# Performance work log

Hardware: AMD Instinct MI355X
Metric: run time of the kernel (lower is better)

Reference implementation:

```python
import jax, jax.numpy as jnp
import numpy as np

D = 4096          # input_dim == output_dim (square FAUST factors)
N = 1024          # batch rows of U
NNZ = 131072      # nonzeros per factor (32 per row)
K = 4             # number of sparse factors


def setup_inputs() -> dict:
    key = jax.random.key(0)
    k_u, k_b, k_v, k_r, k_c = jax.random.split(key, 5)
    U = jax.random.normal(k_u, (N, D), dtype=jnp.float32)
    bias = jax.random.normal(k_b, (D,), dtype=jnp.float32)
    # glorot-ish scaling: ~32 nnz per row -> scale by 1/sqrt(32) for stable chain
    vals = jax.random.normal(k_v, (K, NNZ), dtype=jnp.float32) * (1.0 / np.sqrt(32.0))
    rows = jax.random.randint(k_r, (K, NNZ), 0, D, dtype=jnp.int32)
    cols = jax.random.randint(k_c, (K, NNZ), 0, D, dtype=jnp.int32)
    return {"U": U, "bias": bias, "vals": vals, "rows": rows, "cols": cols}


def _spmm(rows, cols, vals, X):
    # sparse (COO) [D, D] @ dense X [D, N] -> [D, N]
    return jax.ops.segment_sum(vals[:, None] * X[cols], rows, num_segments=D)


def reference(U, bias, vals, rows, cols):
    # torch code applies sparse_matrices[-1] first, then [k-2] ... [0]
    y = U.T  # [D, N]
    for i in range(K - 1, -1, -1):
        y = _spmm(rows[i], cols[i], vals[i], y)
    return y.T + bias  # [N, D]
```

## Files before the change

### kernel.cpp

```cpp
#include <hip/hip_runtime.h>

#define D_DIM 4096
#define N_DIM 1024
#define NNZ_F 131072
#define K_F 4
#define NCHUNK 8
#define LPR 16
#define RPB 16
#define MAXE 1024
#define XS8 (N_DIM / 8)

#define T_TILES ((D_DIM / 64) * (N_DIM / 64))
#define TSTRIDE 132

__device__ __forceinline__ unsigned short f2bf(float f) {
    union { float f; unsigned int u; } v; v.f = f;
    unsigned int r = v.u + 0x7fffu + ((v.u >> 16) & 1u);
    return (unsigned short)(r >> 16);
}
__device__ __forceinline__ float bf_lo(unsigned int w) {
    return __uint_as_float(w << 16);
}
__device__ __forceinline__ float bf_hi_raw(unsigned int w) {
    return __uint_as_float(w);
}

__global__ __launch_bounds__(1024) void fused_t_build_k(const float* __restrict__ in,
                                                        unsigned short* __restrict__ outb,
                                                        const int* __restrict__ rows,
                                                        int* __restrict__ row_ptr_g,
                                                        int* __restrict__ cursor_g,
                                                        int* __restrict__ srow_g) {
    __shared__ int s_cnt[4 * D_DIM];
    __shared__ int s_part[1024];
    const int tid = threadIdx.x;
    const int bid = blockIdx.x;

    if (bid >= K_F) {
        const int tb = bid - K_F;
        float (*tile)[65] = (float (*)[65])s_cnt;
        const int gxi = tb & 63;
        const int gyi = tb >> 6;
        const int c0 = gxi * 64;
        const int r0 = gyi * 64;
        const int tx = tid & 63;
        const int ty = tid >> 6;
#pragma unroll
        for (int i = ty; i < 64; i += 16)
            tile[i][tx] = in[(size_t)(r0 + i) * D_DIM + c0 + tx];
        __syncthreads();
        const int px = (tid & 15) * 4;
        const int py = tid >> 4;
        ushort4 w;
        w.x = f2bf(tile[px + 0][py]);
        w.y = f2bf(tile[px + 1][py]);
        w.z = f2bf(tile[px + 2][py]);
        w.w = f2bf(tile[px + 3][py]);
        *(ushort4*)&outb[(size_t)(c0 + py) * N_DIM + r0 + px] = w;
        return;
    }

    const int f = bid;
    const int grp = (tid >> 8) & 3;
#pragma unroll
    for (int k = 0; k < 16; ++k) s_cnt[tid + k * 1024] = 0;
    __syncthreads();

    int* h = s_cnt + grp * D_DIM;
    const int4* rp4 = (const int4*)(rows + (size_t)f * NNZ_F);
#pragma unroll 4
    for (int it = 0; it < NNZ_F / 4096; ++it) {
        int4 r4 = rp4[(size_t)it * 1024 + tid];
        atomicAdd(&h[r4.x], 1);
        atomicAdd(&h[r4.y], 1);
        atomicAdd(&h[r4.z], 1);
        atomicAdd(&h[r4.w], 1);
    }
    __syncthreads();

    int c[4];
#pragma unroll
    for (int k = 0; k < 4; ++k)
        c[k] = s_cnt[tid * 4 + k] + s_cnt[D_DIM + tid * 4 + k]
             + s_cnt[2 * D_DIM + tid * 4 + k] + s_cnt[3 * D_DIM + tid * 4 + k];
    const int b = tid * 4;

    int* rp   = row_ptr_g + (size_t)f * (D_DIM + 1);
    int* cur  = cursor_g + (size_t)f * D_DIM;
    int* srow = srow_g + (size_t)f * D_DIM;

    if (f == 0) {
        const int part = c[0] + c[1] + c[2] + c[3];
        s_part[tid] = part;
        __syncthreads();
        for (int off = 1; off < 1024; off <<= 1) {
            int v = (tid >= off) ? s_part[tid - off] : 0;
            __syncthreads();
            s_part[tid] += v;
            __syncthreads();
        }
        int excl = s_part[tid] - part;
#pragma unroll
        for (int k = 0; k < 4; ++k) {
            rp[b + k] = excl; cur[b + k] = excl; srow[b + k] = b + k; excl += c[k];
        }
        if (tid == 1023) rp[D_DIM] = NNZ_F;
        return;
    }

    __syncthreads();
    int* hist = s_cnt + 4096;
    int* binc = s_cnt + 4352;
    int* sA   = s_cnt + 4608;
    int* sB   = s_cnt + 4864;
    if (tid < 256) { hist[tid] = 0; binc[tid] = 0; }
    __syncthreads();
#pragma unroll
    for (int k = 0; k < 4; ++k) {
        int l = c[k] > 255 ? 255 : c[k];
        atomicAdd(&hist[l], 1);
    }
    __syncthreads();
    if (tid < 256) { int hv = hist[tid]; sA[tid] = hv; sB[tid] = hv * tid; }
    __syncthreads();
    for (int off = 1; off < 256; off <<= 1) {
        int a = 0, bb = 0;
        if (tid < 256 && tid >= off) { a = sA[tid - off]; bb = sB[tid - off]; }
        __syncthreads();
        if (tid < 256) { sA[tid] += a; sB[tid] += bb; }
        __syncthreads();
    }
#pragma unroll
    for (int k = 0; k < 4; ++k) {
        const int l = c[k] > 255 ? 255 : c[k];
        const int idx = atomicAdd(&binc[l], 1);
        const int pos    = sA[l] - hist[l] + idx;
        const int startp = sB[l] - hist[l] * l + idx * l;
        srow[pos] = b + k;
        rp[pos] = startp;
        cur[b + k] = startp;
    }
    if (tid == 1023) rp[D_DIM] = NNZ_F;
}

__global__ __launch_bounds__(1024) void scatter_all_k(const int* __restrict__ rows,
                                                      const int* __restrict__ cols,
                                                      const float* __restrict__ vals,
                                                      int* __restrict__ cursor,
                                                      uint2* __restrict__ csr) {
    const int f = blockIdx.x >> 5;
    const size_t q = (size_t)(blockIdx.x & 31) * 1024 + threadIdx.x;
    const size_t base = (size_t)f * NNZ_F;
    const int4   r4 = ((const int4*)(rows + base))[q];
    const int4   c4 = ((const int4*)(cols + base))[q];
    const float4 v4 = ((const float4*)(vals + base))[q];
    int* curf = cursor + (size_t)f * D_DIM;
    int p;
    p = atomicAdd(&curf[r4.x], 1);
    csr[base + p] = make_uint2((unsigned)c4.x << 11, __float_as_uint(v4.x));
    p = atomicAdd(&curf[r4.y], 1);
    csr[base + p] = make_uint2((unsigned)c4.y << 11, __float_as_uint(v4.y));
    p = atomicAdd(&curf[r4.z], 1);
    csr[base + p] = make_uint2((unsigned)c4.z << 11, __float_as_uint(v4.z));
    p = atomicAdd(&curf[r4.w], 1);
    csr[base + p] = make_uint2((unsigned)c4.w << 11, __float_as_uint(v4.w));
}

template <bool FINAL>
__global__ __launch_bounds__(256) void spmm_chunk_k(const int* __restrict__ row_ptr,
                                                    const int* __restrict__ sorted_rows,
                                                    const uint2* __restrict__ csr,
                                                    const char* __restrict__ Xb,
                                                    uint4* __restrict__ Y,
                                                    float* __restrict__ out,
                                                    const float* __restrict__ bias) {
    __shared__ float smem[16 * TSTRIDE];
    uint2* s_ent  = (uint2*)smem;
    int*   s_ptr  = (int*)smem + 2048;
    int*   s_srow = (int*)smem + 2072;

    const int tid   = threadIdx.x;
    const int chunk = blockIdx.x & (NCHUNK - 1);
    const int rg    = blockIdx.x >> 3;
    const int r0    = rg * RPB;
    const int sub   = tid >> 4;
    const int lane  = tid & 15;
    const int slot  = chunk * LPR + lane;
    const unsigned sl16 = (unsigned)slot * 16u;

    if (tid <= RPB) s_ptr[tid] = row_ptr[r0 + tid];
    if (tid < RPB)  s_srow[tid] = sorted_rows[r0 + tid];
    __syncthreads();
    const int base  = s_ptr[0];
    const int total = s_ptr[RPB] - base;
    const int start = s_ptr[sub] - base;
    const int end_  = s_ptr[sub + 1] - base;
    const int r     = s_srow[sub];

    float acc[8];
#pragma unroll
    for (int k = 0; k < 8; ++k) acc[k] = 0.f;

    for (int cb2 = 0; cb2 < total; cb2 += MAXE) {
        int cnt = total - cb2;
        if (cnt > MAXE) cnt = MAXE;
        for (int t = tid; t < cnt; t += 256)
            s_ent[t] = csr[base + cb2 + t];
        __syncthreads();
        const int js = start > cb2 ? start : cb2;
        const int je = end_ < cb2 + cnt ? end_ : cb2 + cnt;
        int j = js;
#pragma unroll 2
        for (; j + 1 < je; j += 2) {
            const int j0 = j - cb2;
            const uint2 e0 = s_ent[j0];
            const uint2 e1 = s_ent[j0 + 1];
            const uint4 x0 = *(const uint4*)(Xb + (e0.x + sl16));
            const uint4 x1 = *(const uint4*)(Xb + (e1.x + sl16));
            const float v0 = __uint_as_float(e0.y);
            const float v1 = __uint_as_float(e1.y);
            acc[0] += v0 * bf_lo(x0.x); acc[1] += v0 * bf_hi_raw(x0.x);
            acc[2] += v0 * bf_lo(x0.y); acc[3] += v0 * bf_hi_raw(x0.y);
            acc[4] += v0 * bf_lo(x0.z); acc[5] += v0 * bf_hi_raw(x0.z);
            acc[6] += v0 * bf_lo(x0.w); acc[7] += v0 * bf_hi_raw(x0.w);
            acc[0] += v1 * bf_lo(x1.x); acc[1] += v1 * bf_hi_raw(x1.x);
            acc[2] += v1 * bf_lo(x1.y); acc[3] += v1 * bf_hi_raw(x1.y);
            acc[4] += v1 * bf_lo(x1.z); acc[5] += v1 * bf_hi_raw(x1.z);
            acc[6] += v1 * bf_lo(x1.w); acc[7] += v1 * bf_hi_raw(x1.w);
        }
        if (j < je) {
            const int j0 = j - cb2;
            const uint2 e0 = s_ent[j0];
            const uint4 x0 = *(const uint4*)(Xb + (e0.x + sl16));
            const float v0 = __uint_as_float(e0.y);
            acc[0] += v0 * bf_lo(x0.x); acc[1] += v0 * bf_hi_raw(x0.x);
            acc[2] += v0 * bf_lo(x0.y); acc[3] += v0 * bf_hi_raw(x0.y);
            acc[4] += v0 * bf_lo(x0.z); acc[5] += v0 * bf_hi_raw(x0.z);
            acc[6] += v0 * bf_lo(x0.w); acc[7] += v0 * bf_hi_raw(x0.w);
        }
        __syncthreads();
    }

    if (!FINAL) {
        uint4 o;
        o.x = (unsigned int)f2bf(acc[0]) | ((unsigned int)f2bf(acc[1]) << 16);
        o.y = (unsigned int)f2bf(acc[2]) | ((unsigned int)f2bf(acc[3]) << 16);
        o.z = (unsigned int)f2bf(acc[4]) | ((unsigned int)f2bf(acc[5]) << 16);
        o.w = (unsigned int)f2bf(acc[6]) | ((unsigned int)f2bf(acc[7]) << 16);
        Y[(size_t)r * XS8 + slot] = o;
    } else {
        __syncthreads();
        float* tile = smem;
        const int wbase = sub * TSTRIDE + lane * 8;
        *(float4*)&tile[wbase]     = make_float4(acc[0], acc[1], acc[2], acc[3]);
        *(float4*)&tile[wbase + 4] = make_float4(acc[4], acc[5], acc[6], acc[7]);
        __syncthreads();
        const int n0 = chunk * (N_DIM / NCHUNK);
#pragma unroll
        for (int t = tid; t < 512; t += 256) {
            const int n_loc = t >> 2;
            const int q     = t & 3;
            float4 o;
            o.x = tile[(q * 4 + 0) * TSTRIDE + n_loc];
            o.y = tile[(q * 4 + 1) * TSTRIDE + n_loc];
            o.z = tile[(q * 4 + 2) * TSTRIDE + n_loc];
            o.w = tile[(q * 4 + 3) * TSTRIDE + n_loc];
            const float4 bv = *(const float4*)&bias[r0 + q * 4];
            o.x += bv.x; o.y += bv.y; o.z += bv.z; o.w += bv.w;
            *(float4*)&out[(size_t)(n0 + n_loc) * D_DIM + r0 + q * 4] = o;
        }
    }
}

extern "C" void kernel_launch(void* const* d_in, const int* in_sizes, int n_in,
                              void* d_out, int out_size, void* d_ws, size_t ws_size,
                              hipStream_t stream) {
    const float* U    = (const float*)d_in[0];
    const float* bias = (const float*)d_in[1];
    const float* vals = (const float*)d_in[2];
    const int*   rows = (const int*)d_in[3];
    const int*   cols = (const int*)d_in[4];
    float* out = (float*)d_out;

    char* ws = (char*)d_ws;
    size_t off = 0;
    char* bufA = ws;                   off += (size_t)D_DIM * N_DIM * 2;
    char* bufB = ws + off;             off += (size_t)D_DIM * N_DIM * 2;
    int* row_ptr = (int*)(ws + off);   off += (size_t)K_F * (D_DIM + 1) * 4;
    off = (off + 15) & ~(size_t)15;
    int* cursor  = (int*)(ws + off);   off += (size_t)K_F * D_DIM * 4;
    int* srow    = (int*)(ws + off);   off += (size_t)K_F * D_DIM * 4;
    off = (off + 15) & ~(size_t)15;
    uint2* csr   = (uint2*)(ws + off); off += (size_t)K_F * NNZ_F * 8;

    const int grid_spmm = (D_DIM / RPB) * NCHUNK;

    fused_t_build_k<<<T_TILES + K_F, 1024, 0, stream>>>(
        U, (unsigned short*)bufA, rows, row_ptr, cursor, srow);

    scatter_all_k<<<K_F * (NNZ_F / 4096), 1024, 0, stream>>>(rows, cols, vals, cursor, csr);

    spmm_chunk_k<false><<<grid_spmm, 256, 0, stream>>>(
        row_ptr + 3 * (D_DIM + 1), srow + 3 * D_DIM, csr + 3 * (size_t)NNZ_F,
        (const char*)bufA, (uint4*)bufB, nullptr, nullptr);
    spmm_chunk_k<false><<<grid_spmm, 256, 0, stream>>>(
        row_ptr + 2 * (D_DIM + 1), srow + 2 * D_DIM, csr + 2 * (size_t)NNZ_F,
        (const char*)bufB, (uint4*)bufA, nullptr, nullptr);
    spmm_chunk_k<false><<<grid_spmm, 256, 0, stream>>>(
        row_ptr + 1 * (D_DIM + 1), srow + 1 * D_DIM, csr + 1 * (size_t)NNZ_F,
        (const char*)bufA, (uint4*)bufB, nullptr, nullptr);
    spmm_chunk_k<true><<<grid_spmm, 256, 0, stream>>>(
        row_ptr + 0 * (D_DIM + 1), srow + 0 * D_DIM, csr + 0 * (size_t)NNZ_F,
        (const char*)bufB, nullptr, out, bias);
}
```

Measured before the change: 108.5 us.

## Use per-wavefront row quads with interleaved load balancing in non-final SpMM

For the intermediate SpMM stages, each 64-lane wavefront now handles its own group of 4 sorted rows. It stages that group's CSR entries into a private LDS segment and uses only a wave-local waitcnt, so block-wide __syncthreads barriers are gone. The four wavefronts of a block take quads from mirrored positions in the sorted row order (rg, 511-rg, 512+rg, 1023-rg) to even out the work per block. Quads with more than 512 entries fall back to reading CSR entries straight from global memory. The change relies on lockstep execution within a wavefront for LDS visibility, and it makes LDS use differ between the final and non-final kernel variants.

```diff
diff --git a/kernel.cpp b/kernel.cpp
--- a/kernel.cpp
+++ b/kernel.cpp
@@ -8,6 +8,7 @@
 #define LPR 16
 #define RPB 16
 #define MAXE 1024
+#define SEGE 512
 #define XS8 (N_DIM / 8)
 
 #define T_TILES ((D_DIM / 64) * (N_DIM / 64))
@@ -174,19 +175,101 @@
                                                     uint4* __restrict__ Y,
                                                     float* __restrict__ out,
                                                     const float* __restrict__ bias) {
-    __shared__ float smem[16 * TSTRIDE];
-    uint2* s_ent  = (uint2*)smem;
-    int*   s_ptr  = (int*)smem + 2048;
-    int*   s_srow = (int*)smem + 2072;
+    constexpr int SMEM_BYTES = FINAL ? (16 * TSTRIDE * 4) : (4 * SEGE * 8);
+    __shared__ __align__(16) char smem_raw[SMEM_BYTES];
 
     const int tid   = threadIdx.x;
     const int chunk = blockIdx.x & (NCHUNK - 1);
     const int rg    = blockIdx.x >> 3;
-    const int r0    = rg * RPB;
-    const int sub   = tid >> 4;
     const int lane  = tid & 15;
     const int slot  = chunk * LPR + lane;
     const unsigned sl16 = (unsigned)slot * 16u;
+
+    float acc[8];
+#pragma unroll
+    for (int k = 0; k < 8; ++k) acc[k] = 0.f;
+
+    if (!FINAL) {
+        uint2 (*seg)[SEGE] = (uint2(*)[SEGE])smem_raw;
+        const int wid  = tid >> 6;
+        const int wl   = tid & 63;
+        const int sub4 = (tid >> 4) & 3;
+        int q;
+        switch (wid) {
+            case 0:  q = rg;        break;
+            case 1:  q = 511 - rg;  break;
+            case 2:  q = 512 + rg;  break;
+            default: q = 1023 - rg; break;
+        }
+        const int qb    = q * 4;
+        const int qs    = row_ptr[qb];
+        const int qe    = row_ptr[qb + 4];
+        const int start = row_ptr[qb + sub4];
+        const int end_  = row_ptr[qb + sub4 + 1];
+        const int r     = sorted_rows[qb + sub4];
+        const int total = qe - qs;
+
+        if (total <= SEGE) {
+            for (int t = wl; t < total; t += 64)
+                seg[wid][t] = csr[qs + t];
+            asm volatile("s_waitcnt lgkmcnt(0)" ::: "memory");
+            const uint2* sp = seg[wid];
+            int j = start - qs;
+            const int je = end_ - qs;
+#pragma unroll 2
+            for (; j + 1 < je; j += 2) {
+                const uint2 e0 = sp[j];
+                const uint2 e1 = sp[j + 1];
+                const uint4 x0 = *(const uint4*)(Xb + (e0.x + sl16));
+                const uint4 x1 = *(const uint4*)(Xb + (e1.x + sl16));
+                const float v0 = __uint_as_float(e0.y);
+                const float v1 = __uint_as_float(e1.y);
+                acc[0] += v0 * bf_lo(x0.x); acc[1] += v0 * bf_hi_raw(x0.x);
+                acc[2] += v0 * bf_lo(x0.y); acc[3] += v0 * bf_hi_raw(x0.y);
+                acc[4] += v0 * bf_lo(x0.z); acc[5] += v0 * bf_hi_raw(x0.z);
+                acc[6] += v0 * bf_lo(x0.w); acc[7] += v0 * bf_hi_raw(x0.w);
+                acc[0] += v1 * bf_lo(x1.x); acc[1] += v1 * bf_hi_raw(x1.x);
+                acc[2] += v1 * bf_lo(x1.y); acc[3] += v1 * bf_hi_raw(x1.y);
+                acc[4] += v1 * bf_lo(x1.z); acc[5] += v1 * bf_hi_raw(x1.z);
+                acc[6] += v1 * bf_lo(x1.w); acc[7] += v1 * bf_hi_raw(x1.w);
+            }
+            if (j < je) {
+                const uint2 e0 = sp[j];
+                const uint4 x0 = *(const uint4*)(Xb + (e0.x + sl16));
+                const float v0 = __uint_as_float(e0.y);
+                acc[0] += v0 * bf_lo(x0.x); acc[1] += v0 * bf_hi_raw(x0.x);
+                acc[2] += v0 * bf_lo(x0.y); acc[3] += v0 * bf_hi_raw(x0.y);
+                acc[4] += v0 * bf_lo(x0.z); acc[5] += v0 * bf_hi_raw(x0.z);
+                acc[6] += v0 * bf_lo(x0.w); acc[7] += v0 * bf_hi_raw(x0.w);
+            }
+        } else {
+            for (int j = start; j < end_; ++j) {
+                const uint2 e0 = csr[j];
+                const uint4 x0 = *(const uint4*)(Xb + (e0.x + sl16));
+                const float v0 = __uint_as_float(e0.y);
+                acc[0] += v0 * bf_lo(x0.x); acc[1] += v0 * bf_hi_raw(x0.x);
+                acc[2] += v0 * bf_lo(x0.y); acc[3] += v0 * bf_hi_raw(x0.y);
+                acc[4] += v0 * bf_lo(x0.z); acc[5] += v0 * bf_hi_raw(x0.z);
+                acc[6] += v0 * bf_lo(x0.w); acc[7] += v0 * bf_hi_raw(x0.w);
+            }
+        }
+
+        uint4 o;
+        o.x = (unsigned int)f2bf(acc[0]) | ((unsigned int)f2bf(acc[1]) << 16);
+        o.y = (unsigned int)f2bf(acc[2]) | ((unsigned int)f2bf(acc[3]) << 16);
+        o.z = (unsigned int)f2bf(acc[4]) | ((unsigned int)f2bf(acc[5]) << 16);
+        o.w = (unsigned int)f2bf(acc[6]) | ((unsigned int)f2bf(acc[7]) << 16);
+        Y[(size_t)r * XS8 + slot] = o;
+        return;
+    }
+
+    float* smem   = (float*)smem_raw;
+    uint2* s_ent  = (uint2*)smem_raw;
+    int*   s_ptr  = (int*)smem_raw + 2048;
+    int*   s_srow = (int*)smem_raw + 2072;
+
+    const int r0  = rg * RPB;
+    const int sub = tid >> 4;
 
     if (tid <= RPB) s_ptr[tid] = row_ptr[r0 + tid];
     if (tid < RPB)  s_srow[tid] = sorted_rows[r0 + tid];
@@ -196,10 +279,6 @@
     const int start = s_ptr[sub] - base;
     const int end_  = s_ptr[sub + 1] - base;
     const int r     = s_srow[sub];
-
-    float acc[8];
-#pragma unroll
-    for (int k = 0; k < 8; ++k) acc[k] = 0.f;
 
     for (int cb2 = 0; cb2 < total; cb2 += MAXE) {
         int cnt = total - cb2;
@@ -241,34 +320,25 @@
         __syncthreads();
     }
 
-    if (!FINAL) {
-        uint4 o;
-        o.x = (unsigned int)f2bf(acc[0]) | ((unsigned int)f2bf(acc[1]) << 16);
-        o.y = (unsigned int)f2bf(acc[2]) | ((unsigned int)f2bf(acc[3]) << 16);
-        o.z = (unsigned int)f2bf(acc[4]) | ((unsigned int)f2bf(acc[5]) << 16);
-        o.w = (unsigned int)f2bf(acc[6]) | ((unsigned int)f2bf(acc[7]) << 16);
-        Y[(size_t)r * XS8 + slot] = o;
-    } else {
-        __syncthreads();
-        float* tile = smem;
-        const int wbase = sub * TSTRIDE + lane * 8;
-        *(float4*)&tile[wbase]     = make_float4(acc[0], acc[1], acc[2], acc[3]);
-        *(float4*)&tile[wbase + 4] = make_float4(acc[4], acc[5], acc[6], acc[7]);
-        __syncthreads();
-        const int n0 = chunk * (N_DIM / NCHUNK);
-#pragma unroll
-        for (int t = tid; t < 512; t += 256) {
-            const int n_loc = t >> 2;
-            const int q     = t & 3;
-            float4 o;
-            o.x = tile[(q * 4 + 0) * TSTRIDE + n_loc];
-            o.y = tile[(q * 4 + 1) * TSTRIDE + n_loc];
-            o.z = tile[(q * 4 + 2) * TSTRIDE + n_loc];
-            o.w = tile[(q * 4 + 3) * TSTRIDE + n_loc];
-            const float4 bv = *(const float4*)&bias[r0 + q * 4];
-            o.x += bv.x; o.y += bv.y; o.z += bv.z; o.w += bv.w;
-            *(float4*)&out[(size_t)(n0 + n_loc) * D_DIM + r0 + q * 4] = o;
-        }
+    __syncthreads();
+    float* tile = smem;
+    const int wbase = sub * TSTRIDE + lane * 8;
+    *(float4*)&tile[wbase]     = make_float4(acc[0], acc[1], acc[2], acc[3]);
+    *(float4*)&tile[wbase + 4] = make_float4(acc[4], acc[5], acc[6], acc[7]);
+    __syncthreads();
+    const int n0 = chunk * (N_DIM / NCHUNK);
+#pragma unroll
+    for (int t = tid; t < 512; t += 256) {
+        const int n_loc = t >> 2;
+        const int qd    = t & 3;
+        float4 o;
+        o.x = tile[(qd * 4 + 0) * TSTRIDE + n_loc];
+        o.y = tile[(qd * 4 + 1) * TSTRIDE + n_loc];
+        o.z = tile[(qd * 4 + 2) * TSTRIDE + n_loc];
+        o.w = tile[(qd * 4 + 3) * TSTRIDE + n_loc];
+        const float4 bv = *(const float4*)&bias[r0 + qd * 4];
+        o.x += bv.x; o.y += bv.y; o.z += bv.z; o.w += bv.w;
+        *(float4*)&out[(size_t)(n0 + n_loc) * D_DIM + r0 + qd * 4] = o;
     }
 }
 
```

After: 105.0 us, median of 2. -3.2%, faster.
